# Kernel tuning notes

Measured on AMD Instinct MI355X. Metric: run time of the kernel, lower is better.

## Reference

```python
import jax, jax.numpy as jnp
import numpy as np

B, T, W = 64, 64, 20
VIDEO_DIM = 1024
JOINT_DIM = 1024
K, STRIDE = 4, 4
MARGIN = 0.2
EPS = 1e-8


def _l2norm(x, axis=-1):
    n = jnp.sqrt(jnp.sum(x * x, axis=axis, keepdims=True))
    return x / jnp.maximum(n, EPS)


def _conv1d(x, w, b, stride):
    # x: (B, C, L), w: (O, I, K) -> (B, O, L_out), VALID padding (padding=0)
    y = jax.lax.conv_general_dilated(x, w, (stride,), 'VALID',
                                     dimension_numbers=('NCH', 'OIH', 'NCH'))
    return y + b[None, :, None]


def _diag_loss(scores, margin):
    # faithful port of diag(): row/column margin costs with zeroed diagonal
    b = scores.shape[0]
    d = jnp.diagonal(scores)
    off = 1.0 - jnp.eye(b, dtype=scores.dtype)
    cost_s = jnp.maximum(margin + scores - d[:, None], 0.0) * off
    cost_im = jnp.maximum(margin + scores - d[None, :], 0.0) * off
    return cost_s.sum() / b + cost_im.sum() / b


def setup_inputs() -> dict:
    key = jax.random.key(0)
    ks = jax.random.split(key, 10)
    def g(k, shape, scale=0.02):
        return jax.random.normal(k, shape, dtype=jnp.float32) * scale
    return dict(
        video=jax.random.normal(ks[0], (B, T, VIDEO_DIM), dtype=jnp.float32),
        words=jax.random.normal(ks[1], (B, W, JOINT_DIM), dtype=jnp.float32),
        w_masks=jnp.ones((B, W), dtype=jnp.int32),
        sentences=jax.random.normal(ks[2], (B, JOINT_DIM), dtype=jnp.float32),
        conv0_w=g(ks[3], (JOINT_DIM, VIDEO_DIM, K)),
        conv0_b=jnp.zeros((JOINT_DIM,), jnp.float32),
        conv1_w=g(ks[4], (JOINT_DIM, JOINT_DIM, K)),
        conv1_b=jnp.zeros((JOINT_DIM,), jnp.float32),
        conv2_w=g(ks[5], (JOINT_DIM, JOINT_DIM, K)),
        conv2_b=jnp.zeros((JOINT_DIM,), jnp.float32),
        conv1d_w=g(ks[6], (JOINT_DIM, JOINT_DIM, 1)),
        conv1d_b=jnp.zeros((JOINT_DIM,), jnp.float32),
        fc_w=g(ks[7], (JOINT_DIM, JOINT_DIM)),
        fc_b=jnp.zeros((JOINT_DIM,), jnp.float32),
    )


def reference(video, words, w_masks, sentences,
              conv0_w, conv0_b, conv1_w, conv1_b, conv2_w, conv2_b,
              conv1d_w, conv1d_b, fc_w, fc_b):
    # Vectorizes the original per-sample python loop over the pair axes (i=sentence, j=video).
    x = jnp.transpose(video, (0, 2, 1))          # (B, C, T)
    wmask = (w_masks > 0)                        # (B, W)
    conv_params = [(conv0_w, conv0_b), (conv1_w, conv1_b), (conv2_w, conv2_b)]
    sims = []
    v_tmp = x
    for cw, cb in conv_params:
        v_tmp = jax.nn.relu(_conv1d(v_tmp, cw, cb, STRIDE))
        v = jnp.transpose(_conv1d(v_tmp, conv1d_w, conv1d_b, 1), (0, 2, 1))  # (B, Tl, D)
        # frame_by_word: masked softmax attention of frames over words
        att = jnp.einsum('jtd,iwd->ijtw', v, words)            # (i, j, Tl, W)
        att = jnp.where(wmask[:, None, None, :], att, -1e30)
        att = jax.nn.softmax(att, axis=-1)
        v_s = jnp.einsum('ijtw,iwd->ijtd', att, words)         # attended word ctx
        # cosine sim of l2-normed vectors == dot product
        sim = jnp.einsum('jtd,ijtd->ijt', _l2norm(v), _l2norm(v_s))
        sims.append(sim)
    score_all = jnp.concatenate(sims, axis=2)    # (B, B, T_total=21)
    # torch code sorts descending then means over dim 1 -> mean is sort-invariant
    scores = score_all.mean(axis=2)              # (B, B) local scores
    positive_map = score_all[jnp.arange(B), jnp.arange(B)]     # (B, T_total)
    # global branch: final conv output has length 1 -> squeeze
    g_v = _l2norm(v_tmp[:, :, 0] @ fc_w.T + fc_b)              # (B, D), unit norm
    g_scores = _l2norm(sentences) @ g_v.T                      # [i, j] = cos(g_v[j], sent[i])
    loss = _diag_loss(scores, MARGIN) + _diag_loss(g_scores, MARGIN)
    return loss, positive_map
```

## Files before the change

### kernel.cpp

```cpp
#include <hip/hip_runtime.h>
#include <cmath>
#include <cstdint>


typedef __bf16 bf16_t;
typedef bf16_t bf16x8 __attribute__((ext_vector_type(8)));
typedef bf16_t bf16x4 __attribute__((ext_vector_type(4)));
typedef float  f32x4  __attribute__((ext_vector_type(4)));

__device__ __forceinline__ void gload_lds16(const void* g, void* l) {
    __builtin_amdgcn_global_load_lds(
        (const __attribute__((address_space(1))) void*)g,
        (__attribute__((address_space(3))) void*)l, 16, 0, 0);
}

__device__ __forceinline__ int swz(int r, int c) { return (r * 8 + (c ^ (r & 7))) * 8; }

__device__ __forceinline__ int remap1(int gm) {
    if (gm < 1024) return (gm >> 4) * 21 + (gm & 15);
    if (gm < 1280) { int g = gm - 1024; return (g >> 2) * 21 + 16 + (g & 3); }
    return (gm - 1280) * 21 + 20;
}

__global__ void cast_multi_kernel(
    const float* __restrict__ p0, bf16_t* __restrict__ q0, int n0,
    const float* __restrict__ p1, bf16_t* __restrict__ q1, int n1)
{
    int off = (blockIdx.x * 256 + threadIdx.x) * 4;
    const float* s; bf16_t* d;
    if (off < n0) { s = p0 + off; d = q0 + off; }
    else if ((off -= n0) < n1) { s = p1 + off; d = q1 + off; }
    else return;
    float4 v = *(const float4*)s;
    bf16x4 o = { (bf16_t)v.x, (bf16_t)v.y, (bf16_t)v.z, (bf16_t)v.w };
    *(bf16x4*)d = o;
}

__global__ void transpose_cast_kernel(const float* __restrict__ w, bf16_t* __restrict__ wt) {
    int idx = blockIdx.x * 256 + threadIdx.x;
    int i = idx & 1023;
    int o = idx >> 10;
    float4 v = *(const float4*)(w + ((size_t)o << 12) + (i << 2));
    bf16_t* base = wt + ((size_t)o << 12) + i;
    base[0]    = (bf16_t)v.x;
    base[1024] = (bf16_t)v.y;
    base[2048] = (bf16_t)v.z;
    base[3072] = (bf16_t)v.w;
}

__global__ __launch_bounds__(256) void mgemm_kernel(
    const bf16_t* __restrict__ A, const bf16_t* __restrict__ B,
    const bf16_t* __restrict__ B2, float* __restrict__ CP,
    int N, int K, int Kchunk, int fcTile, int aRow0, int cpSlice)
{
    __shared__ __align__(16) bf16_t sA[2][4096];
    __shared__ __align__(16) bf16_t sB[2][4096];
    const int tid  = threadIdx.x;
    const int lane = tid & 63;
    const int wave = tid >> 6;
    const int bx = blockIdx.x;
    const int m0C = bx * 64;
    int m0A = m0C;
    const bf16_t* Buse = B;
    if (bx == fcTile) { m0A = aRow0; Buse = B2; }
    const int n0 = blockIdx.y * 64;
    const int k0 = blockIdx.z * Kchunk;

    const int sr = tid >> 3;
    const int pc = tid & 7;
    const int lc = pc ^ (sr & 7);
    const bf16_t* Ag = A + (size_t)(m0A + sr) * K + lc * 8;
    const bf16_t* Bg = Buse + (size_t)(n0 + sr) * K + lc * 8;
    const size_t rowskip = (size_t)32 * K;

    const int wr = (wave >> 1) * 32;
    const int wc = (wave & 1) * 32;
    const int fm = lane & 15;
    const int cb = lane >> 4;

    int offA[2][2], offB[2][2];
    #pragma unroll
    for (int h = 0; h < 2; h++) {
        offA[h][0] = swz(wr +      fm, cb + h * 4);
        offA[h][1] = swz(wr + 16 + fm, cb + h * 4);
        offB[h][0] = swz(wc +      fm, cb + h * 4);
        offB[h][1] = swz(wc + 16 + fm, cb + h * 4);
    }

    f32x4 acc[2][2];
    #pragma unroll
    for (int a = 0; a < 2; a++)
        #pragma unroll
        for (int b = 0; b < 2; b++) acc[a][b] = (f32x4){0.f, 0.f, 0.f, 0.f};

    const int nIt = Kchunk >> 6;
    {
        const bf16_t* a = Ag + k0; const bf16_t* b = Bg + k0;
        gload_lds16(a,           &sA[0][tid * 8]);
        gload_lds16(a + rowskip, &sA[0][2048 + tid * 8]);
        gload_lds16(b,           &sB[0][tid * 8]);
        gload_lds16(b + rowskip, &sB[0][2048 + tid * 8]);
    }
    for (int it = 0; it < nIt; ++it) {
        const int buf = it & 1;
        __syncthreads();
        if (it + 1 < nIt) {
            const bf16_t* a = Ag + k0 + (it + 1) * 64;
            const bf16_t* b = Bg + k0 + (it + 1) * 64;
            bf16_t* dA = &sA[buf ^ 1][0];
            bf16_t* dB = &sB[buf ^ 1][0];
            gload_lds16(a,           dA + tid * 8);
            gload_lds16(a + rowskip, dA + 2048 + tid * 8);
            gload_lds16(b,           dB + tid * 8);
            gload_lds16(b + rowskip, dB + 2048 + tid * 8);
        }
        #pragma unroll
        for (int h = 0; h < 2; h++) {
            bf16x8 a0 = *(const bf16x8*)&sA[buf][offA[h][0]];
            bf16x8 a1 = *(const bf16x8*)&sA[buf][offA[h][1]];
            bf16x8 b0 = *(const bf16x8*)&sB[buf][offB[h][0]];
            bf16x8 b1 = *(const bf16x8*)&sB[buf][offB[h][1]];
            acc[0][0] = __builtin_amdgcn_mfma_f32_16x16x32_bf16(a0, b0, acc[0][0], 0, 0, 0);
            acc[0][1] = __builtin_amdgcn_mfma_f32_16x16x32_bf16(a0, b1, acc[0][1], 0, 0, 0);
            acc[1][0] = __builtin_amdgcn_mfma_f32_16x16x32_bf16(a1, b0, acc[1][0], 0, 0, 0);
            acc[1][1] = __builtin_amdgcn_mfma_f32_16x16x32_bf16(a1, b1, acc[1][1], 0, 0, 0);
        }
    }

    float* Cz = CP + (size_t)blockIdx.z * cpSlice;
    #pragma unroll
    for (int im = 0; im < 2; im++)
        #pragma unroll
        for (int rr = 0; rr < 4; rr++) {
            int gm = m0C + wr + im * 16 + (lane >> 4) * 4 + rr;
            #pragma unroll
            for (int in_ = 0; in_ < 2; in_++) {
                int cg = n0 + wc + in_ * 16 + (lane & 15);
                Cz[(size_t)gm * N + cg] = acc[im][in_][rr];
            }
        }
}

__global__ void epilogueB_kernel(const float* __restrict__ CP_, int nz,
    const float* __restrict__ bias, bf16_t* __restrict__ D, float* __restrict__ D2,
    int MN, int N, int relu)
{
    int idx = blockIdx.x * 256 + threadIdx.x;
    if (idx >= MN) return;
    int n = idx % N;
    float s = 0.f;
    for (int z = 0; z < nz; z++) s += CP_[(size_t)z * MN + idx];
    if (bias) s += bias[n];
    if (relu) s = fmaxf(s, 0.f);
    if (D)  D[idx] = (bf16_t)s;
    if (D2) D2[idx] = s;
}

__global__ void epilogueCF_kernel(const float* __restrict__ CP_,
    const float* __restrict__ bias1, const float* __restrict__ biasf,
    bf16_t* __restrict__ VCb, float* __restrict__ GV)
{
    int idx = blockIdx.x * 256 + threadIdx.x;
    int row = idx >> 10, n = idx & 1023;
    float s = CP_[idx] + CP_[idx + 1441792];
    if (row < 1344) VCb[(size_t)remap1(row) * 1024 + n] = (bf16_t)(s + bias1[n]);
    else            GV[(size_t)(row - 1344) * 1024 + n] = s + biasf[n];
}

__global__ void rownorm_kernel(const bf16_t* __restrict__ X, float* __restrict__ nrm, int D) {
    int r = blockIdx.x;
    const bf16_t* x = X + (size_t)r * D;
    float s = 0.f;
    for (int d = threadIdx.x; d < D; d += blockDim.x) { float v = (float)x[d]; s += v * v; }
    #pragma unroll
    for (int o = 32; o; o >>= 1) s += __shfl_xor(s, o, 64);
    __shared__ float red[4];
    if ((threadIdx.x & 63) == 0) red[threadIdx.x >> 6] = s;
    __syncthreads();
    if (threadIdx.x == 0) nrm[r] = sqrtf(red[0] + red[1] + red[2] + red[3]);
}

__global__ void l2normalize2_kernel(const float* __restrict__ X0, float* __restrict__ Y0,
                                    const float* __restrict__ X1, float* __restrict__ Y1,
                                    int D) {
    int r = blockIdx.x & 63;
    const float* x = (blockIdx.x < 64 ? X0 : X1) + (size_t)r * D;
    float*       y = (blockIdx.x < 64 ? Y0 : Y1) + (size_t)r * D;
    float s = 0.f;
    for (int d = threadIdx.x; d < D; d += blockDim.x) { float v = x[d]; s += v * v; }
    #pragma unroll
    for (int o = 32; o; o >>= 1) s += __shfl_xor(s, o, 64);
    __shared__ float red[4];
    __shared__ float tot;
    if ((threadIdx.x & 63) == 0) red[threadIdx.x >> 6] = s;
    __syncthreads();
    if (threadIdx.x == 0) tot = 1.0f / fmaxf(sqrtf(red[0] + red[1] + red[2] + red[3]), 1e-8f);
    __syncthreads();
    float inv = tot;
    for (int d = threadIdx.x; d < D; d += blockDim.x) y[d] = x[d] * inv;
}

__global__ void gram_kernel(const bf16_t* __restrict__ Wb, float* __restrict__ G) {
    int i = blockIdx.x;
    int wave = threadIdx.x >> 6;
    int lane = threadIdx.x & 63;
    int pair = blockIdx.y * 4 + wave;
    int w = pair / 20, w2 = pair % 20;
    const bf16_t* a = Wb + (((size_t)i * 20 + w)  << 10) + lane * 16;
    const bf16_t* b = Wb + (((size_t)i * 20 + w2) << 10) + lane * 16;
    bf16x8 a0 = *(const bf16x8*)a, a1 = *(const bf16x8*)(a + 8);
    bf16x8 b0 = *(const bf16x8*)b, b1 = *(const bf16x8*)(b + 8);
    float s = 0.f;
    #pragma unroll
    for (int e = 0; e < 8; e++)
        s += (float)a0[e] * (float)b0[e] + (float)a1[e] * (float)b1[e];
    #pragma unroll
    for (int o = 32; o; o >>= 1) s += __shfl_xor(s, o, 64);
    if (lane == 0) G[(size_t)i * 400 + pair] = s;
}

__global__ __launch_bounds__(256) void sim_kernel(
    const float* __restrict__ S2, const float* __restrict__ G_,
    const float* __restrict__ VN_, const int* __restrict__ wmask,
    float* __restrict__ SA_)
{
    __shared__ float Gs[400];
    __shared__ float msk[20];
    const int i  = blockIdx.x;
    const int jt = blockIdx.y * 256 + threadIdx.x;
    for (int q = threadIdx.x; q < 400; q += 256) Gs[q] = G_[(size_t)i * 400 + q];
    if (threadIdx.x < 20) msk[threadIdx.x] = (wmask[i * 20 + threadIdx.x] != 0) ? 1.f : 0.f;
    __syncthreads();
    if (jt >= 1344) return;

    float s[20], p[20];
    float mx = -1e30f;
    #pragma unroll
    for (int w = 0; w < 20; w++) {
        s[w] = S2[(size_t)(i * 20 + w) * 1344 + jt];
        if (msk[w] != 0.f) mx = fmaxf(mx, s[w]);
    }
    float denom = 0.f, num = 0.f;
    #pragma unroll
    for (int w = 0; w < 20; w++) {
        p[w] = (msk[w] != 0.f) ? __expf(s[w] - mx) : 0.f;
        denom += p[w];
        num   += p[w] * s[w];
    }
    float quad = 0.f;
    #pragma unroll
    for (int w = 0; w < 20; w++) {
        float c = 0.f;
        #pragma unroll
        for (int w2 = 0; w2 < 20; w2++) c += Gs[w * 20 + w2] * p[w2];
        quad += p[w] * c;
    }
    float dot = num / denom;
    float vsn = sqrtf(fmaxf(quad, 0.f)) / denom;
    float sim = dot / (fmaxf(VN_[jt], 1e-8f) * fmaxf(vsn, 1e-8f));
    SA_[(size_t)i * 1344 + jt] = sim;
}

__global__ void scores_kernel(const float* __restrict__ SA_, float* __restrict__ SC_,
                              float* __restrict__ out) {
    int idx = blockIdx.x * 256 + threadIdx.x;
    int i = idx >> 6, j = idx & 63;
    const float* row = SA_ + (size_t)idx * 21;
    float s = 0.f;
    #pragma unroll
    for (int t = 0; t < 21; t++) s += row[t];
    SC_[idx] = s * (1.0f / 21.0f);
    if (i == j) {
        #pragma unroll
        for (int t = 0; t < 21; t++) out[1 + i * 21 + t] = row[t];
    }
}

__global__ void gscore_kernel(const float* __restrict__ SN_, const float* __restrict__ GN_,
                              float* __restrict__ GS_) {
    int item = blockIdx.x * 4 + (threadIdx.x >> 6);
    int i = item >> 6, j = item & 63;
    int lane = threadIdx.x & 63;
    const float* a = SN_ + (size_t)i * 1024;
    const float* b = GN_ + (size_t)j * 1024;
    float s = 0.f;
    #pragma unroll
    for (int q = 0; q < 16; q++) { int d = lane + 64 * q; s += a[d] * b[d]; }
    #pragma unroll
    for (int o = 32; o; o >>= 1) s += __shfl_xor(s, o, 64);
    if (lane == 0) GS_[item] = s;
}

__global__ void loss_kernel(const float* __restrict__ SC_, const float* __restrict__ GS_,
                            float* __restrict__ out) {
    __shared__ float d1[64], d2[64], red[4];
    int tid = threadIdx.x;
    if (tid < 64) { d1[tid] = SC_[tid * 65]; d2[tid] = GS_[tid * 65]; }
    __syncthreads();
    float acc = 0.f;
    for (int idx = tid; idx < 4096; idx += 256) {
        int i = idx >> 6, j = idx & 63;
        if (i != j) {
            float s = SC_[idx];
            acc += fmaxf(0.2f + s - d1[i], 0.f) + fmaxf(0.2f + s - d1[j], 0.f);
            float g = GS_[idx];
            acc += fmaxf(0.2f + g - d2[i], 0.f) + fmaxf(0.2f + g - d2[j], 0.f);
        }
    }
    #pragma unroll
    for (int o = 32; o; o >>= 1) acc += __shfl_xor(acc, o, 64);
    if ((tid & 63) == 0) red[tid >> 6] = acc;
    __syncthreads();
    if (tid == 0) out[0] = (red[0] + red[1] + red[2] + red[3]) * (1.0f / 64.0f);
}

extern "C" void kernel_launch(void* const* d_in, const int* in_sizes, int n_in,
                              void* d_out, int out_size, void* d_ws, size_t ws_size,
                              hipStream_t stream)
{
    const float* video     = (const float*)d_in[0];
    const float* words     = (const float*)d_in[1];
    const int*   w_masks   = (const int*)  d_in[2];
    const float* sentences = (const float*)d_in[3];
    const float* conv0_w   = (const float*)d_in[4];
    const float* conv0_b   = (const float*)d_in[5];
    const float* conv1_w   = (const float*)d_in[6];
    const float* conv1_b   = (const float*)d_in[7];
    const float* conv2_w   = (const float*)d_in[8];
    const float* conv2_b   = (const float*)d_in[9];
    const float* conv1d_w  = (const float*)d_in[10];
    const float* conv1d_b  = (const float*)d_in[11];
    const float* fc_w      = (const float*)d_in[12];
    const float* fc_b      = (const float*)d_in[13];
    float* out = (float*)d_out;
    float* ws = (float*)d_ws;

    bf16_t* WTb    = (bf16_t*)(ws + 0);
    float*  S2     = ws + 0;
    float*  VN     = ws + 1720320;
    float*  GR     = ws + 1721664;
    float*  SA     = ws + 1747264;
    float*  SC     = ws + 1833280;
    float*  GV     = ws + 1837376;
    float*  GN     = ws + 1902912;
    float*  SN     = ws + 1968448;
    float*  GS     = ws + 2033984;
    bf16_t* Vb     = (bf16_t*)(ws + 2097152);
    float*  CP0    = ws + 4194304;
    bf16_t* C1b    = (bf16_t*)(ws + 2097152);
    bf16_t* Fb     = (bf16_t*)(ws + 2621440);
    float*  CP1    = ws + 4194304;
    float*  CP2    = ws + 4194304;
    float*  CPcf   = ws + 3145728;
    bf16_t* Astack = (bf16_t*)(ws + 6291456);
    bf16_t* VCb    = (bf16_t*)(ws + 6979584);
    bf16_t* Wordsb = (bf16_t*)(ws + 7667712);

    bf16_t* A2b = Astack + 1048576;
    bf16_t* A3b = Astack + 1310720;

    dim3 blk(256);

    cast_multi_kernel<<<5376, blk, 0, stream>>>(video, Vb, 4194304, words, Wordsb, 1310720);

    transpose_cast_kernel<<<4096, blk, 0, stream>>>(conv0_w, WTb);
    mgemm_kernel<<<dim3(16,16,2), blk, 0, stream>>>(
        Vb, WTb, nullptr, CP0, 1024, 4096, 2048, -1, 0, 1048576);
    epilogueB_kernel<<<4096, blk, 0, stream>>>(CP0, 2, conv0_b, Astack, nullptr, 1048576, 1024, 1);

    cast_multi_kernel<<<2048, blk, 0, stream>>>(conv1d_w, C1b, 1048576, fc_w, Fb, 1048576);

    transpose_cast_kernel<<<4096, blk, 0, stream>>>(conv1_w, WTb);
    mgemm_kernel<<<dim3(4,16,8), blk, 0, stream>>>(
        Astack, WTb, nullptr, CP1, 1024, 4096, 512, -1, 0, 262144);
    epilogueB_kernel<<<1024, blk, 0, stream>>>(CP1, 8, conv1_b, A2b, nullptr, 262144, 1024, 1);

    transpose_cast_kernel<<<4096, blk, 0, stream>>>(conv2_w, WTb);
    mgemm_kernel<<<dim3(1,16,16), blk, 0, stream>>>(
        A2b, WTb, nullptr, CP2, 1024, 4096, 256, -1, 0, 65536);
    epilogueB_kernel<<<256, blk, 0, stream>>>(CP2, 16, conv2_b, A3b, nullptr, 65536, 1024, 1);

    mgemm_kernel<<<dim3(22,16,2), blk, 0, stream>>>(
        Astack, C1b, Fb, CPcf, 1024, 1024, 512, 21, 1280, 1441792);
    epilogueCF_kernel<<<5632, blk, 0, stream>>>(CPcf, conv1d_b, fc_b, VCb, GV);

    mgemm_kernel<<<dim3(20,21,1), blk, 0, stream>>>(
        Wordsb, VCb, nullptr, S2, 1344, 1024, 1024, -1, 0, 0);

    rownorm_kernel<<<1344, blk, 0, stream>>>(VCb, VN, 1024);
    gram_kernel<<<dim3(64,100), blk, 0, stream>>>(Wordsb, GR);
    sim_kernel<<<dim3(64,6), blk, 0, stream>>>(S2, GR, VN, w_masks, SA);
    scores_kernel<<<16, blk, 0, stream>>>(SA, SC, out);
    l2normalize2_kernel<<<128, blk, 0, stream>>>(GV, GN, sentences, SN, 1024);
    gscore_kernel<<<1024, blk, 0, stream>>>(SN, GN, GS);
    loss_kernel<<<1, blk, 0, stream>>>(SC, GS, out);
}
```

Measured before the change: 258.4 us.

## Merge prep/cast/norm kernels and deepen split-K across all GEMMs

All weight transposes and input casts are folded into one prep kernel with separate workspace buffers, which cuts launch count. Rownorm and gram are fused, and so are scores and l2normalize. Split-K depth is doubled for every GEMM, and the attention GEMM now uses split-K with its two partials summed in sim_kernel. The aim is more parallelism in the small-M GEMMs and fewer launches, at the cost of more partial-sum traffic in the epilogues.

```diff
diff --git a/kernel.cpp b/kernel.cpp
--- a/kernel.cpp
+++ b/kernel.cpp
@@ -22,30 +22,40 @@
     return (gm - 1280) * 21 + 20;
 }
 
-__global__ void cast_multi_kernel(
-    const float* __restrict__ p0, bf16_t* __restrict__ q0, int n0,
-    const float* __restrict__ p1, bf16_t* __restrict__ q1, int n1)
-{
-    int off = (blockIdx.x * 256 + threadIdx.x) * 4;
-    const float* s; bf16_t* d;
-    if (off < n0) { s = p0 + off; d = q0 + off; }
-    else if ((off -= n0) < n1) { s = p1 + off; d = q1 + off; }
-    else return;
-    float4 v = *(const float4*)s;
-    bf16x4 o = { (bf16_t)v.x, (bf16_t)v.y, (bf16_t)v.z, (bf16_t)v.w };
-    *(bf16x4*)d = o;
-}
-
-__global__ void transpose_cast_kernel(const float* __restrict__ w, bf16_t* __restrict__ wt) {
-    int idx = blockIdx.x * 256 + threadIdx.x;
-    int i = idx & 1023;
-    int o = idx >> 10;
-    float4 v = *(const float4*)(w + ((size_t)o << 12) + (i << 2));
-    bf16_t* base = wt + ((size_t)o << 12) + i;
-    base[0]    = (bf16_t)v.x;
-    base[1024] = (bf16_t)v.y;
-    base[2048] = (bf16_t)v.z;
-    base[3072] = (bf16_t)v.w;
+__global__ void prep_kernel(
+    const float* __restrict__ c0w, const float* __restrict__ c1w,
+    const float* __restrict__ c2w,
+    bf16_t* __restrict__ WT0, bf16_t* __restrict__ WT1, bf16_t* __restrict__ WT2,
+    const float* __restrict__ video, bf16_t* __restrict__ Vb,
+    const float* __restrict__ words, bf16_t* __restrict__ Wordsb,
+    const float* __restrict__ c1dw, bf16_t* __restrict__ C1b,
+    const float* __restrict__ fcw, bf16_t* __restrict__ Fb)
+{
+    int bx = blockIdx.x;
+    if (bx < 12288) {
+        const float* w; bf16_t* wt;
+        if (bx < 4096)      { w = c0w; wt = WT0; }
+        else if (bx < 8192) { w = c1w; wt = WT1; bx -= 4096; }
+        else                { w = c2w; wt = WT2; bx -= 8192; }
+        int idx = bx * 256 + threadIdx.x;
+        int i = idx & 1023, o = idx >> 10;
+        float4 v = *(const float4*)(w + ((size_t)o << 12) + (i << 2));
+        bf16_t* base = wt + ((size_t)o << 12) + i;
+        base[0]    = (bf16_t)v.x;
+        base[1024] = (bf16_t)v.y;
+        base[2048] = (bf16_t)v.z;
+        base[3072] = (bf16_t)v.w;
+    } else {
+        const float* s; bf16_t* d;
+        if (bx < 16384)      { s = video; d = Vb;     bx -= 12288; }
+        else if (bx < 17664) { s = words; d = Wordsb; bx -= 16384; }
+        else if (bx < 18688) { s = c1dw;  d = C1b;    bx -= 17664; }
+        else                 { s = fcw;   d = Fb;     bx -= 18688; }
+        int off = (bx * 256 + threadIdx.x) * 4;
+        float4 v = *(const float4*)(s + off);
+        bf16x4 o4 = { (bf16_t)v.x, (bf16_t)v.y, (bf16_t)v.z, (bf16_t)v.w };
+        *(bf16x4*)(d + off) = o4;
+    }
 }
 
 __global__ __launch_bounds__(256) void mgemm_kernel(
@@ -142,8 +152,7 @@
 }
 
 __global__ void epilogueB_kernel(const float* __restrict__ CP_, int nz,
-    const float* __restrict__ bias, bf16_t* __restrict__ D, float* __restrict__ D2,
-    int MN, int N, int relu)
+    const float* __restrict__ bias, bf16_t* __restrict__ D, int MN, int N, int relu)
 {
     int idx = blockIdx.x * 256 + threadIdx.x;
     if (idx >= MN) return;
@@ -152,8 +161,7 @@
     for (int z = 0; z < nz; z++) s += CP_[(size_t)z * MN + idx];
     if (bias) s += bias[n];
     if (relu) s = fmaxf(s, 0.f);
-    if (D)  D[idx] = (bf16_t)s;
-    if (D2) D2[idx] = s;
+    D[idx] = (bf16_t)s;
 }
 
 __global__ void epilogueCF_kernel(const float* __restrict__ CP_,
@@ -162,65 +170,47 @@
 {
     int idx = blockIdx.x * 256 + threadIdx.x;
     int row = idx >> 10, n = idx & 1023;
-    float s = CP_[idx] + CP_[idx + 1441792];
+    float s = CP_[idx] + CP_[idx + 1441792] + CP_[idx + 2 * 1441792] + CP_[idx + 3 * 1441792];
     if (row < 1344) VCb[(size_t)remap1(row) * 1024 + n] = (bf16_t)(s + bias1[n]);
     else            GV[(size_t)(row - 1344) * 1024 + n] = s + biasf[n];
 }
 
-__global__ void rownorm_kernel(const bf16_t* __restrict__ X, float* __restrict__ nrm, int D) {
-    int r = blockIdx.x;
-    const bf16_t* x = X + (size_t)r * D;
-    float s = 0.f;
-    for (int d = threadIdx.x; d < D; d += blockDim.x) { float v = (float)x[d]; s += v * v; }
-    #pragma unroll
-    for (int o = 32; o; o >>= 1) s += __shfl_xor(s, o, 64);
-    __shared__ float red[4];
-    if ((threadIdx.x & 63) == 0) red[threadIdx.x >> 6] = s;
-    __syncthreads();
-    if (threadIdx.x == 0) nrm[r] = sqrtf(red[0] + red[1] + red[2] + red[3]);
-}
-
-__global__ void l2normalize2_kernel(const float* __restrict__ X0, float* __restrict__ Y0,
-                                    const float* __restrict__ X1, float* __restrict__ Y1,
-                                    int D) {
-    int r = blockIdx.x & 63;
-    const float* x = (blockIdx.x < 64 ? X0 : X1) + (size_t)r * D;
-    float*       y = (blockIdx.x < 64 ? Y0 : Y1) + (size_t)r * D;
-    float s = 0.f;
-    for (int d = threadIdx.x; d < D; d += blockDim.x) { float v = x[d]; s += v * v; }
-    #pragma unroll
-    for (int o = 32; o; o >>= 1) s += __shfl_xor(s, o, 64);
-    __shared__ float red[4];
-    __shared__ float tot;
-    if ((threadIdx.x & 63) == 0) red[threadIdx.x >> 6] = s;
-    __syncthreads();
-    if (threadIdx.x == 0) tot = 1.0f / fmaxf(sqrtf(red[0] + red[1] + red[2] + red[3]), 1e-8f);
-    __syncthreads();
-    float inv = tot;
-    for (int d = threadIdx.x; d < D; d += blockDim.x) y[d] = x[d] * inv;
-}
-
-__global__ void gram_kernel(const bf16_t* __restrict__ Wb, float* __restrict__ G) {
-    int i = blockIdx.x;
-    int wave = threadIdx.x >> 6;
-    int lane = threadIdx.x & 63;
-    int pair = blockIdx.y * 4 + wave;
-    int w = pair / 20, w2 = pair % 20;
-    const bf16_t* a = Wb + (((size_t)i * 20 + w)  << 10) + lane * 16;
-    const bf16_t* b = Wb + (((size_t)i * 20 + w2) << 10) + lane * 16;
-    bf16x8 a0 = *(const bf16x8*)a, a1 = *(const bf16x8*)(a + 8);
-    bf16x8 b0 = *(const bf16x8*)b, b1 = *(const bf16x8*)(b + 8);
-    float s = 0.f;
-    #pragma unroll
-    for (int e = 0; e < 8; e++)
-        s += (float)a0[e] * (float)b0[e] + (float)a1[e] * (float)b1[e];
-    #pragma unroll
-    for (int o = 32; o; o >>= 1) s += __shfl_xor(s, o, 64);
-    if (lane == 0) G[(size_t)i * 400 + pair] = s;
+__global__ void normgram_kernel(const bf16_t* __restrict__ VCb, float* __restrict__ VN,
+                                const bf16_t* __restrict__ Wb, float* __restrict__ G)
+{
+    int bx = blockIdx.x;
+    if (bx < 1344) {
+        const bf16_t* x = VCb + ((size_t)bx << 10);
+        float s = 0.f;
+        for (int d = threadIdx.x; d < 1024; d += 256) { float v = (float)x[d]; s += v * v; }
+        #pragma unroll
+        for (int o = 32; o; o >>= 1) s += __shfl_xor(s, o, 64);
+        __shared__ float red[4];
+        if ((threadIdx.x & 63) == 0) red[threadIdx.x >> 6] = s;
+        __syncthreads();
+        if (threadIdx.x == 0) VN[bx] = sqrtf(red[0] + red[1] + red[2] + red[3]);
+    } else {
+        int g = bx - 1344;
+        int i = g / 100, piece = g % 100;
+        int wave = threadIdx.x >> 6, lane = threadIdx.x & 63;
+        int pair = piece * 4 + wave;
+        int w = pair / 20, w2 = pair % 20;
+        const bf16_t* a = Wb + (((size_t)i * 20 + w)  << 10) + lane * 16;
+        const bf16_t* b = Wb + (((size_t)i * 20 + w2) << 10) + lane * 16;
+        bf16x8 a0 = *(const bf16x8*)a, a1 = *(const bf16x8*)(a + 8);
+        bf16x8 b0 = *(const bf16x8*)b, b1 = *(const bf16x8*)(b + 8);
+        float s = 0.f;
+        #pragma unroll
+        for (int e = 0; e < 8; e++)
+            s += (float)a0[e] * (float)b0[e] + (float)a1[e] * (float)b1[e];
+        #pragma unroll
+        for (int o = 32; o; o >>= 1) s += __shfl_xor(s, o, 64);
+        if (lane == 0) G[(size_t)i * 400 + pair] = s;
+    }
 }
 
 __global__ __launch_bounds__(256) void sim_kernel(
-    const float* __restrict__ S2, const float* __restrict__ G_,
+    const float* __restrict__ CPat, const float* __restrict__ G_,
     const float* __restrict__ VN_, const int* __restrict__ wmask,
     float* __restrict__ SA_)
 {
@@ -237,7 +227,8 @@
     float mx = -1e30f;
     #pragma unroll
     for (int w = 0; w < 20; w++) {
-        s[w] = S2[(size_t)(i * 20 + w) * 1344 + jt];
+        size_t q = (size_t)(i * 20 + w) * 1344 + jt;
+        s[w] = CPat[q] + CPat[q + 1720320];
         if (msk[w] != 0.f) mx = fmaxf(mx, s[w]);
     }
     float denom = 0.f, num = 0.f;
@@ -261,18 +252,41 @@
     SA_[(size_t)i * 1344 + jt] = sim;
 }
 
-__global__ void scores_kernel(const float* __restrict__ SA_, float* __restrict__ SC_,
-                              float* __restrict__ out) {
-    int idx = blockIdx.x * 256 + threadIdx.x;
-    int i = idx >> 6, j = idx & 63;
-    const float* row = SA_ + (size_t)idx * 21;
-    float s = 0.f;
-    #pragma unroll
-    for (int t = 0; t < 21; t++) s += row[t];
-    SC_[idx] = s * (1.0f / 21.0f);
-    if (i == j) {
-        #pragma unroll
-        for (int t = 0; t < 21; t++) out[1 + i * 21 + t] = row[t];
+__global__ void scores_l2_kernel(const float* __restrict__ SA_, float* __restrict__ SC_,
+                                 float* __restrict__ out,
+                                 const float* __restrict__ GV, float* __restrict__ GN,
+                                 const float* __restrict__ sent, float* __restrict__ SN)
+{
+    int bx = blockIdx.x;
+    if (bx < 16) {
+        int idx = bx * 256 + threadIdx.x;
+        int i = idx >> 6, j = idx & 63;
+        const float* row = SA_ + (size_t)idx * 21;
+        float s = 0.f;
+        #pragma unroll
+        for (int t = 0; t < 21; t++) s += row[t];
+        SC_[idx] = s * (1.0f / 21.0f);
+        if (i == j) {
+            #pragma unroll
+            for (int t = 0; t < 21; t++) out[1 + i * 21 + t] = row[t];
+        }
+    } else {
+        int b2 = bx - 16;
+        int r = b2 & 63;
+        const float* x = (b2 < 64 ? GV : sent) + ((size_t)r << 10);
+        float*       y = (b2 < 64 ? GN : SN)   + ((size_t)r << 10);
+        float s = 0.f;
+        for (int d = threadIdx.x; d < 1024; d += 256) { float v = x[d]; s += v * v; }
+        #pragma unroll
+        for (int o = 32; o; o >>= 1) s += __shfl_xor(s, o, 64);
+        __shared__ float red[4];
+        __shared__ float tot;
+        if ((threadIdx.x & 63) == 0) red[threadIdx.x >> 6] = s;
+        __syncthreads();
+        if (threadIdx.x == 0) tot = 1.0f / fmaxf(sqrtf(red[0] + red[1] + red[2] + red[3]), 1e-8f);
+        __syncthreads();
+        float inv = tot;
+        for (int d = threadIdx.x; d < 1024; d += 256) y[d] = x[d] * inv;
     }
 }
 
@@ -335,63 +349,60 @@
     float* out = (float*)d_out;
     float* ws = (float*)d_ws;
 
-    bf16_t* WTb    = (bf16_t*)(ws + 0);
-    float*  S2     = ws + 0;
-    float*  VN     = ws + 1720320;
-    float*  GR     = ws + 1721664;
-    float*  SA     = ws + 1747264;
-    float*  SC     = ws + 1833280;
-    float*  GV     = ws + 1837376;
-    float*  GN     = ws + 1902912;
-    float*  SN     = ws + 1968448;
-    float*  GS     = ws + 2033984;
-    bf16_t* Vb     = (bf16_t*)(ws + 2097152);
-    float*  CP0    = ws + 4194304;
-    bf16_t* C1b    = (bf16_t*)(ws + 2097152);
-    bf16_t* Fb     = (bf16_t*)(ws + 2621440);
-    float*  CP1    = ws + 4194304;
-    float*  CP2    = ws + 4194304;
-    float*  CPcf   = ws + 3145728;
-    bf16_t* Astack = (bf16_t*)(ws + 6291456);
-    bf16_t* VCb    = (bf16_t*)(ws + 6979584);
-    bf16_t* Wordsb = (bf16_t*)(ws + 7667712);
+    bf16_t* WT0    = (bf16_t*)(ws + 0);
+    bf16_t* WT1    = (bf16_t*)(ws + 2097152);
+    bf16_t* WT2    = (bf16_t*)(ws + 4194304);
+    bf16_t* Vb     = (bf16_t*)(ws + 6291456);
+    bf16_t* Wordsb = (bf16_t*)(ws + 8388608);
+    bf16_t* C1b    = (bf16_t*)(ws + 9043968);
+    bf16_t* Fb     = (bf16_t*)(ws + 9568256);
+    bf16_t* Astack = (bf16_t*)(ws + 10092544);
+    bf16_t* VCb    = (bf16_t*)(ws + 10780672);
+    float*  CP0    = ws + 11468800;
+    float*  CP1    = ws + 15663104;
+    float*  CP2    = ws + 19857408;
+    float*  CPcf   = ws + 21954560;
+    float*  CPat   = ws + 27721728;
+    float*  VN     = ws + 31162368;
+    float*  GR     = ws + 31163712;
+    float*  SA     = ws + 31189312;
+    float*  SC     = ws + 31275328;
+    float*  GV     = ws + 31279424;
+    float*  GN     = ws + 31344960;
+    float*  SN     = ws + 31410496;
+    float*  GS     = ws + 31476032;
 
     bf16_t* A2b = Astack + 1048576;
     bf16_t* A3b = Astack + 1310720;
 
     dim3 blk(256);
 
-    cast_multi_kernel<<<5376, blk, 0, stream>>>(video, Vb, 4194304, words, Wordsb, 1310720);
-
-    transpose_cast_kernel<<<4096, blk, 0, stream>>>(conv0_w, WTb);
-    mgemm_kernel<<<dim3(16,16,2), blk, 0, stream>>>(
-        Vb, WTb, nullptr, CP0, 1024, 4096, 2048, -1, 0, 1048576);
-    epilogueB_kernel<<<4096, blk, 0, stream>>>(CP0, 2, conv0_b, Astack, nullptr, 1048576, 1024, 1);
-
-    cast_multi_kernel<<<2048, blk, 0, stream>>>(conv1d_w, C1b, 1048576, fc_w, Fb, 1048576);
-
-    transpose_cast_kernel<<<4096, blk, 0, stream>>>(conv1_w, WTb);
-    mgemm_kernel<<<dim3(4,16,8), blk, 0, stream>>>(
-        Astack, WTb, nullptr, CP1, 1024, 4096, 512, -1, 0, 262144);
-    epilogueB_kernel<<<1024, blk, 0, stream>>>(CP1, 8, conv1_b, A2b, nullptr, 262144, 1024, 1);
-
-    transpose_cast_kernel<<<4096, blk, 0, stream>>>(conv2_w, WTb);
-    mgemm_kernel<<<dim3(1,16,16), blk, 0, stream>>>(
-        A2b, WTb, nullptr, CP2, 1024, 4096, 256, -1, 0, 65536);
-    epilogueB_kernel<<<256, blk, 0, stream>>>(CP2, 16, conv2_b, A3b, nullptr, 65536, 1024, 1);
-
-    mgemm_kernel<<<dim3(22,16,2), blk, 0, stream>>>(
-        Astack, C1b, Fb, CPcf, 1024, 1024, 512, 21, 1280, 1441792);
+    prep_kernel<<<19712, blk, 0, stream>>>(
+        conv0_w, conv1_w, conv2_w, WT0, WT1, WT2,
+        video, Vb, words, Wordsb, conv1d_w, C1b, fc_w, Fb);
+
+    mgemm_kernel<<<dim3(16,16,4), blk, 0, stream>>>(
+        Vb, WT0, nullptr, CP0, 1024, 4096, 1024, -1, 0, 1048576);
+    epilogueB_kernel<<<4096, blk, 0, stream>>>(CP0, 4, conv0_b, Astack, 1048576, 1024, 1);
+
+    mgemm_kernel<<<dim3(4,16,16), blk, 0, stream>>>(
+        Astack, WT1, nullptr, CP1, 1024, 4096, 256, -1, 0, 262144);
+    epilogueB_kernel<<<1024, blk, 0, stream>>>(CP1, 16, conv1_b, A2b, 262144, 1024, 1);
+
+    mgemm_kernel<<<dim3(1,16,32), blk, 0, stream>>>(
+        A2b, WT2, nullptr, CP2, 1024, 4096, 128, -1, 0, 65536);
+    epilogueB_kernel<<<256, blk, 0, stream>>>(CP2, 32, conv2_b, A3b, 65536, 1024, 1);
+
+    mgemm_kernel<<<dim3(22,16,4), blk, 0, stream>>>(
+        Astack, C1b, Fb, CPcf, 1024, 1024, 256, 21, 1280, 1441792);
     epilogueCF_kernel<<<5632, blk, 0, stream>>>(CPcf, conv1d_b, fc_b, VCb, GV);
 
-    mgemm_kernel<<<dim3(20,21,1), blk, 0, stream>>>(
-        Wordsb, VCb, nullptr, S2, 1344, 1024, 1024, -1, 0, 0);
-
-    rownorm_kernel<<<1344, blk, 0, stream>>>(VCb, VN, 1024);
-    gram_kernel<<<dim3(64,100), blk, 0, stream>>>(Wordsb, GR);
-    sim_kernel<<<dim3(64,6), blk, 0, stream>>>(S2, GR, VN, w_masks, SA);
-    scores_kernel<<<16, blk, 0, stream>>>(SA, SC, out);
-    l2normalize2_kernel<<<128, blk, 0, stream>>>(GV, GN, sentences, SN, 1024);
+    mgemm_kernel<<<dim3(20,21,2), blk, 0, stream>>>(
+        Wordsb, VCb, nullptr, CPat, 1344, 1024, 512, -1, 0, 1720320);
+
+    normgram_kernel<<<7744, blk, 0, stream>>>(VCb, VN, Wordsb, GR);
+    sim_kernel<<<dim3(64,6), blk, 0, stream>>>(CPat, GR, VN, w_masks, SA);
+    scores_l2_kernel<<<144, blk, 0, stream>>>(SA, SC, out, GV, GN, sentences, SN);
     gscore_kernel<<<1024, blk, 0, stream>>>(SN, GN, GS);
     loss_kernel<<<1, blk, 0, stream>>>(SC, GS, out);
 }
```

Result: faster. 242.8 us (-6.0%).
